# Kernel tuning notes

Measured on AMD Instinct MI355X. Metric: run time of the kernel, lower is better.

## Reference

```python
import math
import jax, jax.numpy as jnp
import numpy as np

N_FLOWS = 5
DIM = 64
NH = 128          # hidden multiplier -> hidden width = DIM*NH = 8192
BATCH = 4096


def _masks(out_f, in_f, dim):
    od, idd = out_f // dim, in_f // dim
    mask_d = np.zeros((out_f, in_f), np.float32)
    mask_o = np.ones((out_f, in_f), np.float32)
    for i in range(dim):
        mask_d[i * od:(i + 1) * od, i * idd:(i + 1) * idd] = 1.0
        mask_o[i * od:(i + 1) * od, i * idd:] = 0.0
    return jnp.asarray(mask_d), jnp.asarray(mask_o)

MASK_D1, MASK_O1 = _masks(DIM * NH, DIM, DIM)   # layer 1: (H, D)
MASK_D2, MASK_O2 = _masks(DIM, DIM * NH, DIM)   # layer 2: (D, H)


def masked_weight(x, W, dw, b, mask_d, mask_o, dim, grad=None):
    """MaskedWeight.forward. W:(out,in), dw:(out,1), b:(out,)."""
    out_f, in_f = W.shape
    od, idd = out_f // dim, in_f // dim
    w = jnp.exp(W) * mask_d + W * mask_o                 # (out, in)
    wsn = jnp.sum(w * w, axis=-1, keepdims=True)         # (out, 1)
    wn = jnp.exp(dw) * w / jnp.sqrt(wsn)                 # weight-normalized
    wpl = dw + W - 0.5 * jnp.log(wsn)                    # (out, in)
    # extract diagonal blocks of wpl^T: (dim, idd, od)
    blocks = wpl.reshape(dim, od, dim, idd)
    wpl_t = blocks[np.arange(dim), :, np.arange(dim), :].transpose(0, 2, 1)
    y = x @ wn.T + b                                     # (B, out)
    g = wpl_t.transpose(0, 2, 1)                         # (dim, od, idd)
    if grad is None:
        new_grad = jnp.broadcast_to(g[None], (x.shape[0],) + g.shape)
    else:
        # logsumexp over contracted block axis: out (B, dim, od, b_prev)
        new_grad = jax.nn.logsumexp(
            g[None, :, :, None, :] + jnp.swapaxes(grad, -2, -1)[:, :, None, :, :],
            axis=-1)
    return y, new_grad


def tanh_layer(x, grad):
    g = -2.0 * (x - math.log(2.0) + jax.nn.softplus(-2.0 * x))
    return jnp.tanh(x), g.reshape(grad.shape) + grad


def bnaf_flow(x, W1, d1, b1, W2, d2, b2, gate):
    h, g = masked_weight(x, W1, d1, b1, MASK_D1, MASK_O1, DIM)
    h, g = tanh_layer(h, g)
    y, g = masked_weight(h, W2, d2, b2, MASK_D2, MASK_O2, DIM, grad=g)
    grad = g[:, :, 0, 0]                                  # (B, DIM) -- squeeze
    if gate is None:                                      # res=None (last flow)
        return y, jnp.sum(grad, axis=-1)
    s = jax.nn.sigmoid(gate)                              # res='gated'
    out = s * y + (1.0 - s) * x
    ld = jnp.sum(jax.nn.softplus(grad + gate) - jax.nn.softplus(gate), axis=-1)
    return out, ld


def setup_inputs() -> dict:
    key = jax.random.key(0)
    ks = jax.random.split(key, 8)
    H = DIM * NH
    return {
        "x":  jax.random.normal(ks[0], (BATCH, DIM), jnp.float32),
        "W1": jax.random.normal(ks[1], (N_FLOWS, H, DIM), jnp.float32) * 0.1,
        "d1": jax.random.normal(ks[2], (N_FLOWS, H, 1), jnp.float32) * 0.1,
        "b1": jax.random.normal(ks[3], (N_FLOWS, H), jnp.float32) * 0.01,
        "W2": jax.random.normal(ks[4], (N_FLOWS, DIM, H), jnp.float32) * 0.1,
        "d2": jax.random.normal(ks[5], (N_FLOWS, DIM, 1), jnp.float32) * 0.1,
        "b2": jax.random.normal(ks[6], (N_FLOWS, DIM), jnp.float32) * 0.01,
        "gates": jax.random.normal(ks[7], (N_FLOWS - 1,), jnp.float32),
    }


def reference(x, W1, d1, b1, W2, d2, b2, gates):
    log_det = jnp.zeros(x.shape[0], x.dtype)
    for f in range(N_FLOWS):
        gate = gates[f] if f < N_FLOWS - 1 else None
        x, ld = bnaf_flow(x, W1[f], d1[f], b1[f], W2[f], d2[f], b2[f], gate)
        log_det = log_det + ld
        if f < N_FLOWS - 1:                               # Permutation 'flip'
            x = x[:, ::-1]
    return x, log_det
```

## Files before the change

### kernel.cpp

```cpp
#include <hip/hip_runtime.h>
#include <hip/hip_bf16.h>
#include <math.h>

#define NFLOWS 5
#define DIMF 64
#define HID 8192
#define BATCHN 4096

typedef unsigned int u32;
typedef __bf16 bf16x8 __attribute__((ext_vector_type(8)));
typedef float f32x4 __attribute__((ext_vector_type(4)));

__device__ __forceinline__ short f2bf_s(float x){
  u32 b = __float_as_uint(x);
  b += 0x7fff + ((b >> 16) & 1);
  return (short)(b >> 16);
}
__device__ __forceinline__ float softplus_f(float z){
  return fmaxf(z, 0.f) + log1pf(__expf(-fabsf(z)));
}

__global__ __launch_bounds__(256) void prep1_kernel(
    const float* __restrict__ W1, const float* __restrict__ d1,
    short* __restrict__ wn1s, float* __restrict__ g1)
{
  int w = threadIdx.x >> 6;
  int k = threadIdx.x & 63;
  int R = blockIdx.x * 4 + w;
  int rl = R & (HID - 1);
  int blk = rl >> 7;
  float Wv = W1[(size_t)R * DIMF + k];
  float wv;
  if (k == blk)      wv = __expf(Wv);
  else if (k < blk)  wv = Wv;
  else               wv = 0.f;
  float sq = wv * wv;
  #pragma unroll
  for (int m = 1; m < 64; m <<= 1) sq += __shfl_xor(sq, m, 64);
  float d1v = d1[R];
  float sc = __expf(d1v) * rsqrtf(sq);
  int f   = R >> 13;
  int i   = rl >> 7;
  int rem = rl & 127;
  int nt  = rem >> 4;
  int n16 = rem & 15;
  int ks2 = k >> 5;
  int q   = (k & 31) >> 3;
  int j   = k & 7;
  size_t dst = ((((size_t)(f * 64 + i) * 8 + nt) * 2 + ks2) << 9)
             + ((q * 16 + n16) << 3) + j;
  wn1s[dst] = f2bf_s(wv * sc);
  if (k == blk) g1[R] = d1v + Wv - 0.5f * __logf(sq);
}

__global__ __launch_bounds__(256) void prep2_kernel(
    const float* __restrict__ W2, const float* __restrict__ d2,
    const float* __restrict__ g1,
    short* __restrict__ wn2s, float* __restrict__ expc4,
    float* __restrict__ cmax)
{
  __shared__ float red[256];
  int f = blockIdx.x >> 6;
  int iRow = blockIdx.x & 63;
  int tid = threadIdx.x;
  const float* Wrow = W2 + ((size_t)(f * DIMF + iRow)) * HID;
  float d2v = d2[f * DIMF + iRow];
  float part = 0.f;
  for (int k = tid; k < HID; k += 256) {
    float Wv = Wrow[k];
    int kb = k >> 7;
    float wv = (kb == iRow) ? __expf(Wv) : ((kb < iRow) ? Wv : 0.f);
    part += wv * wv;
  }
  red[tid] = part; __syncthreads();
  for (int s = 128; s > 0; s >>= 1) {
    if (tid < s) red[tid] += red[tid + s];
    __syncthreads();
  }
  float wsn = red[0];
  __syncthreads();
  float ls = __logf(wsn);
  float sc = __expf(d2v) * rsqrtf(wsn);
  float lmax = -1e30f;
  int kheld = -1; float cvheld = 0.f;
  int nt2 = iRow >> 4, c16r = iRow & 15;
  for (int k = tid; k < HID; k += 256) {
    float Wv = Wrow[k];
    int kb = k >> 7;
    float wv = (kb == iRow) ? __expf(Wv) : ((kb < iRow) ? Wv : 0.f);
    int i = k >> 7, ks = (k >> 5) & 3, q = (k >> 3) & 3, j = k & 7;
    size_t dst = ((((size_t)(f * 64 + i) * 4 + ks) * 4 + nt2) << 9)
               + ((q * 16 + c16r) << 3) + j;
    wn2s[dst] = f2bf_s(wv * sc);
    if (kb == iRow) {
      float cv = g1[f * HID + k] + d2v + Wv - 0.5f * ls;
      cvheld = cv; kheld = k;
      lmax = fmaxf(lmax, cv);
    }
  }
  red[tid] = lmax; __syncthreads();
  for (int s = 128; s > 0; s >>= 1) {
    if (tid < s) red[tid] = fmaxf(red[tid], red[tid + s]);
    __syncthreads();
  }
  float M = red[0];
  if (kheld >= 0) expc4[f * HID + kheld] = 4.f * __expf(cvheld - M);
  if (tid == 0) cmax[f * DIMF + iRow] = M;
}

__global__ __launch_bounds__(1024, 4) void bnaf_main_kernel(
    const float* __restrict__ x_in,
    const float* __restrict__ b1, const float* __restrict__ b2,
    const float* __restrict__ gates,
    const short* __restrict__ wn1s,
    const short* __restrict__ wn2s,
    const float* __restrict__ expc4, const float* __restrict__ cmax,
    float* __restrict__ out)
{
  __shared__ __attribute__((aligned(16))) char smem[77184];
  float* xs  = (float*)smem;
  short* xbS = (short*)(smem + 4352);
  float* ldp = (float*)(smem + 76160);

  const int tid  = threadIdx.x;
  const int w    = tid >> 6;
  const int lane = tid & 63;
  const int c16  = lane & 15;
  const int q    = lane >> 4;
  const int r0   = blockIdx.x * 16;

  short* tsw = (short*)(smem + 6528 + w * 4352);

  for (int e = tid; e < 1024; e += 1024) {
    int row = e >> 6, col = e & 63;
    float v = x_in[((size_t)(r0 + row) << 6) | col];
    xs[row * 68 + col] = v;
    xbS[(col >> 3) * 136 + row * 8 + (col & 7)] = f2bf_s(v);
  }
  float ldtot = 0.f;
  __syncthreads();

  #pragma unroll 1
  for (int f = 0; f < NFLOWS; ++f) {
    const float gatev = (f < NFLOWS - 1) ? gates[f] : 0.f;
    const float spg   = (f < NFLOWS - 1) ? softplus_f(gatev) : 0.f;

    const bf16x8 xa0 = *(const bf16x8*)(xbS + q * 136 + c16 * 8);
    const bf16x8 xa1 = *(const bf16x8*)(xbS + (4 + q) * 136 + c16 * 8);

    f32x4 yacc[4];
    #pragma unroll
    for (int n = 0; n < 4; ++n) yacc[n] = f32x4{0.f, 0.f, 0.f, 0.f};
    float ldacc[4] = {0.f, 0.f, 0.f, 0.f};

    #pragma unroll 1
    for (int ii = 0; ii < 4; ++ii) {
      const int i = ii * 16 + w;

      const short* p1l = wn1s + (((size_t)(f * 64 + i)) << 13) + lane * 8;
      f32x4 d[8];
      #pragma unroll
      for (int nt = 0; nt < 8; ++nt) {
        bf16x8 bw0 = *(const bf16x8*)(p1l + nt * 1024);
        bf16x8 bw1 = *(const bf16x8*)(p1l + nt * 1024 + 512);
        f32x4 z = {0.f, 0.f, 0.f, 0.f};
        z = __builtin_amdgcn_mfma_f32_16x16x32_bf16(xa0, bw0, z, 0, 0, 0);
        d[nt] = __builtin_amdgcn_mfma_f32_16x16x32_bf16(xa1, bw1, z, 0, 0, 0);
      }

      const int hb = f * HID + i * 128 + c16;
      float sacc[4] = {0.f, 0.f, 0.f, 0.f};
      #pragma unroll
      for (int nt = 0; nt < 8; ++nt) {
        float b1v = b1[hb + nt * 16];
        float ec4 = expc4[hb + nt * 16];
        #pragma unroll
        for (int r = 0; r < 4; ++r) {
          float h = d[nt][r] + b1v;
          h = fminf(fmaxf(h, -30.f), 30.f);
          float u = __expf(2.f * h);
          float v = __builtin_amdgcn_rcpf(u + 1.f);
          float t = fmaf(-2.f, v, 1.f);
          sacc[r] = fmaf(ec4 * u, v * v, sacc[r]);
          tsw[(nt * 2 + (c16 >> 3)) * 136 + (q * 4 + r) * 8 + (c16 & 7)] = f2bf_s(t);
        }
      }
      asm volatile("s_waitcnt lgkmcnt(0)" ::: "memory");

      #pragma unroll
      for (int m = 1; m < 16; m <<= 1) {
        #pragma unroll
        for (int r = 0; r < 4; ++r) sacc[r] += __shfl_xor(sacc[r], m, 64);
      }
      const float Mi = cmax[f * DIMF + i];
      #pragma unroll
      for (int r = 0; r < 4; ++r) {
        float grad = Mi + __logf(sacc[r]);
        ldacc[r] += (f < NFLOWS - 1) ? (softplus_f(grad + gatev) - spg) : grad;
      }

      const short* p2l = wn2s + (((size_t)(f * 64 + i)) << 13) + lane * 8;
      #pragma unroll
      for (int ks = 0; ks < 4; ++ks) {
        bf16x8 ta = *(const bf16x8*)(tsw + (ks * 4 + q) * 136 + c16 * 8);
        #pragma unroll
        for (int nt2 = 0; nt2 < 4; ++nt2) {
          bf16x8 wb = *(const bf16x8*)(p2l + (ks * 4 + nt2) * 512);
          yacc[nt2] = __builtin_amdgcn_mfma_f32_16x16x32_bf16(ta, wb, yacc[nt2], 0, 0, 0);
        }
      }
    }

    asm volatile("s_waitcnt lgkmcnt(0)" ::: "memory");
    float* ypw = (float*)(smem + 6528 + w * 4352);
    #pragma unroll
    for (int nt2 = 0; nt2 < 4; ++nt2)
      #pragma unroll
      for (int r = 0; r < 4; ++r)
        ypw[(nt2 * 4 + r) * 64 + lane] = yacc[nt2][r];
    if (c16 == 0) {
      #pragma unroll
      for (int r = 0; r < 4; ++r) ldp[w * 16 + q * 4 + r] = ldacc[r];
    }
    __syncthreads();

    float sgate = 0.f;
    if (f < NFLOWS - 1) sgate = __builtin_amdgcn_rcpf(1.f + __expf(-gatev));
    int row = tid >> 6, col = tid & 63;
    int li  = (col & 15) | ((row & 12) << 2);
    int idx = ((col >> 4) * 4 + (row & 3)) * 64 + li;
    float v = b2[f * DIMF + col];
    #pragma unroll
    for (int ww = 0; ww < 16; ++ww)
      v += ((const float*)(smem + 6528 + ww * 4352))[idx];
    float nx = 0.f; int nrow = 0, ncol = 0;
    if (f < NFLOWS - 1) {
      float xv = xs[row * 68 + col];
      nx = fmaf(sgate, v - xv, xv);
      nrow = row; ncol = 63 - col;
    } else {
      out[((size_t)(r0 + row) << 6) | col] = v;
    }
    if (tid < 16) {
      float a = 0.f;
      #pragma unroll
      for (int ww = 0; ww < 16; ++ww) a += ldp[ww * 16 + tid];
      ldtot += a;
    }
    __syncthreads();
    if (f < NFLOWS - 1) {
      xs[nrow * 68 + ncol] = nx;
      xbS[(ncol >> 3) * 136 + nrow * 8 + (ncol & 7)] = f2bf_s(nx);
      __syncthreads();
    }
  }

  if (tid < 16) out[(size_t)BATCHN * DIMF + r0 + tid] = ldtot;
}

extern "C" void kernel_launch(void* const* d_in, const int* in_sizes, int n_in,
                              void* d_out, int out_size, void* d_ws, size_t ws_size,
                              hipStream_t stream)
{
  const float* x     = (const float*)d_in[0];
  const float* W1    = (const float*)d_in[1];
  const float* d1    = (const float*)d_in[2];
  const float* b1    = (const float*)d_in[3];
  const float* W2    = (const float*)d_in[4];
  const float* d2    = (const float*)d_in[5];
  const float* b2    = (const float*)d_in[6];
  const float* gates = (const float*)d_in[7];
  float* out = (float*)d_out;

  char* ws = (char*)d_ws;
  short* wn1s  = (short*)ws;
  short* wn2s  = (short*)(ws + 5242880);
  float* expc4 = (float*)(ws + 10485760);
  float* cmaxp = (float*)(ws + 10649600);
  float* g1    = (float*)(ws + 10650880);

  hipLaunchKernelGGL(prep1_kernel, dim3(10240), dim3(256), 0, stream, W1, d1, wn1s, g1);
  hipLaunchKernelGGL(prep2_kernel, dim3(320), dim3(256), 0, stream, W2, d2, g1, wn2s, expc4, cmaxp);
  hipLaunchKernelGGL(bnaf_main_kernel, dim3(256), dim3(1024), 0, stream,
                     x, b1, b2, gates, wn1s, wn2s, expc4, cmaxp, out);
}
```

Baseline: 285.6 us.

## Skip masked-zero MFMA tiles and transpose MFMA operands for packed stores

The main kernel now skips MFMA work on weight tiles that the autoregressive mask makes zero. The second K-half of layer 1 runs only for blocks i>=32, and layer-2 output tiles below the block index are skipped. MFMA operand order is swapped so each lane holds four contiguous hidden units. This allows float4 loads of b1/expc4, packed bf16 stores of the tanh outputs, and a shorter shuffle reduction. prep2 also moves to 1024 threads with an unrolled loop, and the final gather index is changed to match the transposed accumulator layout. Divergent per-wave work (the branches depend on i) may cause imbalance across waves.

Result: no change. 284.5 us (-0.4%).

```diff
diff --git a/kernel.cpp b/kernel.cpp
--- a/kernel.cpp
+++ b/kernel.cpp
@@ -15,6 +15,17 @@
   u32 b = __float_as_uint(x);
   b += 0x7fff + ((b >> 16) & 1);
   return (short)(b >> 16);
+}
+__device__ __forceinline__ u32 pk_bf16(float a, float b){
+#if __has_builtin(__builtin_amdgcn_cvt_pk_bf16_f32)
+  typedef __bf16 bf16x2_t __attribute__((ext_vector_type(2)));
+  bf16x2_t r = __builtin_amdgcn_cvt_pk_bf16_f32(a, b);
+  return __builtin_bit_cast(u32, r);
+#else
+  u32 x = __float_as_uint(a); x += 0x7fff + ((x >> 16) & 1);
+  u32 y = __float_as_uint(b); y += 0x7fff + ((y >> 16) & 1);
+  return (x >> 16) | (y & 0xffff0000u);
+#endif
 }
 __device__ __forceinline__ float softplus_f(float z){
   return fmaxf(z, 0.f) + log1pf(__expf(-fabsf(z)));
@@ -53,27 +64,29 @@
   if (k == blk) g1[R] = d1v + Wv - 0.5f * __logf(sq);
 }
 
-__global__ __launch_bounds__(256) void prep2_kernel(
+__global__ __launch_bounds__(1024) void prep2_kernel(
     const float* __restrict__ W2, const float* __restrict__ d2,
     const float* __restrict__ g1,
     short* __restrict__ wn2s, float* __restrict__ expc4,
     float* __restrict__ cmax)
 {
-  __shared__ float red[256];
+  __shared__ float red[1024];
   int f = blockIdx.x >> 6;
   int iRow = blockIdx.x & 63;
   int tid = threadIdx.x;
   const float* Wrow = W2 + ((size_t)(f * DIMF + iRow)) * HID;
   float d2v = d2[f * DIMF + iRow];
   float part = 0.f;
-  for (int k = tid; k < HID; k += 256) {
+  #pragma unroll
+  for (int kk = 0; kk < 8; ++kk) {
+    int k = tid + kk * 1024;
     float Wv = Wrow[k];
     int kb = k >> 7;
     float wv = (kb == iRow) ? __expf(Wv) : ((kb < iRow) ? Wv : 0.f);
     part += wv * wv;
   }
   red[tid] = part; __syncthreads();
-  for (int s = 128; s > 0; s >>= 1) {
+  for (int s = 512; s > 0; s >>= 1) {
     if (tid < s) red[tid] += red[tid + s];
     __syncthreads();
   }
@@ -83,13 +96,15 @@
   float sc = __expf(d2v) * rsqrtf(wsn);
   float lmax = -1e30f;
   int kheld = -1; float cvheld = 0.f;
-  int nt2 = iRow >> 4, c16r = iRow & 15;
-  for (int k = tid; k < HID; k += 256) {
+  int mt2 = iRow >> 4, c16r = iRow & 15;
+  #pragma unroll
+  for (int kk = 0; kk < 8; ++kk) {
+    int k = tid + kk * 1024;
     float Wv = Wrow[k];
     int kb = k >> 7;
     float wv = (kb == iRow) ? __expf(Wv) : ((kb < iRow) ? Wv : 0.f);
     int i = k >> 7, ks = (k >> 5) & 3, q = (k >> 3) & 3, j = k & 7;
-    size_t dst = ((((size_t)(f * 64 + i) * 4 + ks) * 4 + nt2) << 9)
+    size_t dst = ((((size_t)(f * 64 + i) * 4 + ks) * 4 + mt2) << 9)
                + ((q * 16 + c16r) << 3) + j;
     wn2s[dst] = f2bf_s(wv * sc);
     if (kb == iRow) {
@@ -99,7 +114,7 @@
     }
   }
   red[tid] = lmax; __syncthreads();
-  for (int s = 128; s > 0; s >>= 1) {
+  for (int s = 512; s > 0; s >>= 1) {
     if (tid < s) red[tid] = fmaxf(red[tid], red[tid + s]);
     __syncthreads();
   }
@@ -131,8 +146,8 @@
 
   short* tsw = (short*)(smem + 6528 + w * 4352);
 
-  for (int e = tid; e < 1024; e += 1024) {
-    int row = e >> 6, col = e & 63;
+  {
+    int row = tid >> 6, col = tid & 63;
     float v = x_in[((size_t)(r0 + row) << 6) | col];
     xs[row * 68 + col] = v;
     xbS[(col >> 3) * 136 + row * 8 + (col & 7)] = f2bf_s(v);
@@ -151,7 +166,7 @@
     f32x4 yacc[4];
     #pragma unroll
     for (int n = 0; n < 4; ++n) yacc[n] = f32x4{0.f, 0.f, 0.f, 0.f};
-    float ldacc[4] = {0.f, 0.f, 0.f, 0.f};
+    float ldacc = 0.f;
 
     #pragma unroll 1
     for (int ii = 0; ii < 4; ++ii) {
@@ -162,51 +177,58 @@
       #pragma unroll
       for (int nt = 0; nt < 8; ++nt) {
         bf16x8 bw0 = *(const bf16x8*)(p1l + nt * 1024);
-        bf16x8 bw1 = *(const bf16x8*)(p1l + nt * 1024 + 512);
         f32x4 z = {0.f, 0.f, 0.f, 0.f};
-        z = __builtin_amdgcn_mfma_f32_16x16x32_bf16(xa0, bw0, z, 0, 0, 0);
-        d[nt] = __builtin_amdgcn_mfma_f32_16x16x32_bf16(xa1, bw1, z, 0, 0, 0);
+        d[nt] = __builtin_amdgcn_mfma_f32_16x16x32_bf16(bw0, xa0, z, 0, 0, 0);
       }
-
-      const int hb = f * HID + i * 128 + c16;
-      float sacc[4] = {0.f, 0.f, 0.f, 0.f};
+      if (i >= 32) {
+        #pragma unroll
+        for (int nt = 0; nt < 8; ++nt) {
+          bf16x8 bw1 = *(const bf16x8*)(p1l + nt * 1024 + 512);
+          d[nt] = __builtin_amdgcn_mfma_f32_16x16x32_bf16(bw1, xa1, d[nt], 0, 0, 0);
+        }
+      }
+
+      const float* b1p = b1    + f * HID + i * 128 + q * 4;
+      const float* ecp = expc4 + f * HID + i * 128 + q * 4;
+      float sacc = 0.f;
       #pragma unroll
       for (int nt = 0; nt < 8; ++nt) {
-        float b1v = b1[hb + nt * 16];
-        float ec4 = expc4[hb + nt * 16];
+        float4 b1q = *(const float4*)(b1p + nt * 16);
+        float4 ecq = *(const float4*)(ecp + nt * 16);
+        float t[4];
         #pragma unroll
         for (int r = 0; r < 4; ++r) {
-          float h = d[nt][r] + b1v;
+          float bb = (r == 0) ? b1q.x : (r == 1) ? b1q.y : (r == 2) ? b1q.z : b1q.w;
+          float ee = (r == 0) ? ecq.x : (r == 1) ? ecq.y : (r == 2) ? ecq.z : ecq.w;
+          float h = d[nt][r] + bb;
           h = fminf(fmaxf(h, -30.f), 30.f);
           float u = __expf(2.f * h);
           float v = __builtin_amdgcn_rcpf(u + 1.f);
-          float t = fmaf(-2.f, v, 1.f);
-          sacc[r] = fmaf(ec4 * u, v * v, sacc[r]);
-          tsw[(nt * 2 + (c16 >> 3)) * 136 + (q * 4 + r) * 8 + (c16 & 7)] = f2bf_s(t);
+          t[r] = fmaf(-2.f, v, 1.f);
+          sacc = fmaf(ee * u, v * v, sacc);
         }
+        uint2 pk; pk.x = pk_bf16(t[0], t[1]); pk.y = pk_bf16(t[2], t[3]);
+        *(uint2*)(tsw + c16 * 136 + nt * 16 + q * 4) = pk;
       }
       asm volatile("s_waitcnt lgkmcnt(0)" ::: "memory");
 
-      #pragma unroll
-      for (int m = 1; m < 16; m <<= 1) {
+      sacc += __shfl_xor(sacc, 16, 64);
+      sacc += __shfl_xor(sacc, 32, 64);
+      const float Mi = cmax[f * DIMF + i];
+      float grad = Mi + __logf(sacc);
+      ldacc += (f < NFLOWS - 1) ? (softplus_f(grad + gatev) - spg) : grad;
+
+      const short* p2l = wn2s + (((size_t)(f * 64 + i)) << 13) + lane * 8;
+      const int mt0 = i >> 4;
+      #pragma unroll
+      for (int ks = 0; ks < 4; ++ks) {
+        bf16x8 tb = *(const bf16x8*)(tsw + c16 * 136 + ks * 32 + q * 8);
         #pragma unroll
-        for (int r = 0; r < 4; ++r) sacc[r] += __shfl_xor(sacc[r], m, 64);
-      }
-      const float Mi = cmax[f * DIMF + i];
-      #pragma unroll
-      for (int r = 0; r < 4; ++r) {
-        float grad = Mi + __logf(sacc[r]);
-        ldacc[r] += (f < NFLOWS - 1) ? (softplus_f(grad + gatev) - spg) : grad;
-      }
-
-      const short* p2l = wn2s + (((size_t)(f * 64 + i)) << 13) + lane * 8;
-      #pragma unroll
-      for (int ks = 0; ks < 4; ++ks) {
-        bf16x8 ta = *(const bf16x8*)(tsw + (ks * 4 + q) * 136 + c16 * 8);
-        #pragma unroll
-        for (int nt2 = 0; nt2 < 4; ++nt2) {
-          bf16x8 wb = *(const bf16x8*)(p2l + (ks * 4 + nt2) * 512);
-          yacc[nt2] = __builtin_amdgcn_mfma_f32_16x16x32_bf16(ta, wb, yacc[nt2], 0, 0, 0);
+        for (int mt = 0; mt < 4; ++mt) {
+          if (mt >= mt0) {
+            bf16x8 wb = *(const bf16x8*)(p2l + (ks * 4 + mt) * 512);
+            yacc[mt] = __builtin_amdgcn_mfma_f32_16x16x32_bf16(wb, tb, yacc[mt], 0, 0, 0);
+          }
         }
       }
     }
@@ -214,21 +236,17 @@
     asm volatile("s_waitcnt lgkmcnt(0)" ::: "memory");
     float* ypw = (float*)(smem + 6528 + w * 4352);
     #pragma unroll
-    for (int nt2 = 0; nt2 < 4; ++nt2)
+    for (int mt = 0; mt < 4; ++mt)
       #pragma unroll
       for (int r = 0; r < 4; ++r)
-        ypw[(nt2 * 4 + r) * 64 + lane] = yacc[nt2][r];
-    if (c16 == 0) {
-      #pragma unroll
-      for (int r = 0; r < 4; ++r) ldp[w * 16 + q * 4 + r] = ldacc[r];
-    }
+        ypw[(mt * 4 + r) * 64 + lane] = yacc[mt][r];
+    if (q == 0) ldp[w * 16 + c16] = ldacc;
     __syncthreads();
 
     float sgate = 0.f;
     if (f < NFLOWS - 1) sgate = __builtin_amdgcn_rcpf(1.f + __expf(-gatev));
     int row = tid >> 6, col = tid & 63;
-    int li  = (col & 15) | ((row & 12) << 2);
-    int idx = ((col >> 4) * 4 + (row & 3)) * 64 + li;
+    int idx = (((col >> 4) * 4 + (col & 3)) * 64) + (((col >> 2) & 3) * 16) + row;
     float v = b2[f * DIMF + col];
     #pragma unroll
     for (int ww = 0; ww < 16; ++ww)
@@ -280,7 +298,7 @@
   float* g1    = (float*)(ws + 10650880);
 
   hipLaunchKernelGGL(prep1_kernel, dim3(10240), dim3(256), 0, stream, W1, d1, wn1s, g1);
-  hipLaunchKernelGGL(prep2_kernel, dim3(320), dim3(256), 0, stream, W2, d2, g1, wn2s, expc4, cmaxp);
+  hipLaunchKernelGGL(prep2_kernel, dim3(320), dim3(1024), 0, stream, W2, d2, g1, wn2s, expc4, cmaxp);
   hipLaunchKernelGGL(bnaf_main_kernel, dim3(256), dim3(1024), 0, stream,
                      x, b1, b2, gates, wn1s, wn2s, expc4, cmaxp, out);
 }
```
